# Kernel optimization log

Measured on AMD Instinct MI355X. Metric: run time of the kernel, lower is better.

The kernel has to match this reference:

```python
import jax, jax.numpy as jnp
import numpy as np

N_NODES = 100_000
N_EDGES = 1_200_000
D = 64


def setup_inputs() -> dict:
    key = jax.random.key(0)
    k1, k2, k3, k4, k5 = jax.random.split(key, 5)
    feat = jax.random.normal(k1, (N_NODES, D), dtype=jnp.float32)
    feat_0 = jax.random.normal(k2, (N_NODES, D), dtype=jnp.float32)
    std = 1.0 / np.sqrt(D)  # reset_parameters: uniform(-std, std), std = 1/sqrt(out_size)
    weight = jax.random.uniform(k3, (D, D), dtype=jnp.float32, minval=-std, maxval=std)
    src = jax.random.randint(k4, (N_EDGES,), 0, N_NODES, dtype=jnp.int32)
    dst = jax.random.randint(k5, (N_EDGES,), 0, N_NODES, dtype=jnp.int32)
    return {
        "feat": feat,
        "feat_0": feat_0,
        "weight": weight,
        "src": src,
        "dst": dst,
        "alpha": jnp.float32(0.1),
        "lamda": jnp.float32(0.5),
        "layer": 1,
    }


def reference(feat, feat_0, weight, src, dst, alpha, lamda, layer):
    # beta = log(lamda / layer + 1)
    beta = jnp.log(lamda / layer + 1.0)
    # in-degrees from destination endpoints, clamped at 1 (as in DGL path)
    degs = jax.ops.segment_sum(
        jnp.ones_like(dst, dtype=feat.dtype), dst, num_segments=N_NODES
    )
    norm = jnp.maximum(degs, 1.0) ** -0.5  # [N]
    norm = norm[:, None]  # [N, 1]
    # symmetric degree-normalized SpMM: D^{-1/2} A D^{-1/2} X via copy_u + sum
    h = feat * norm
    h = jax.ops.segment_sum(h[src], dst, num_segments=N_NODES)  # scatter-add over edges
    h = h * norm
    # GCNII combination: initial residual + identity mapping
    feat_sum = h * (1.0 - alpha) + feat_0 * alpha
    rst = (1.0 - beta) * feat_sum + beta * (feat_sum @ weight)
    return rst
```

## Files before the change

kernel.cpp:

```cpp
#include <hip/hip_runtime.h>
#include <hip/hip_fp16.h>

#define DDIM 64
#define MAXNS 2048
#define PART_TPB 256
#define PART_EPT 16
#define PART_EPB (PART_TPB * PART_EPT)

__device__ __forceinline__ float atomAddF(float* p, float v) {
    return unsafeAtomicAdd(p, v);
}


__global__ void slice_count_kernel(const int* __restrict__ dst, int* __restrict__ sliceCnt,
                                   int nE, int NS) {
    __shared__ int lh[MAXNS];
    int t = threadIdx.x;
    int blockBase = blockIdx.x * PART_EPB;
    for (int i = t; i < NS; i += PART_TPB) lh[i] = 0;
    __syncthreads();
    #pragma unroll
    for (int c = 0; c < 4; ++c) {
        int e0 = blockBase + (c * PART_TPB + t) * 4;
        if (e0 + 3 < nE) {
            int4 b = *(const int4*)(dst + e0);
            atomicAdd(&lh[b.x >> 8], 1); atomicAdd(&lh[b.y >> 8], 1);
            atomicAdd(&lh[b.z >> 8], 1); atomicAdd(&lh[b.w >> 8], 1);
        } else {
            for (int j = 0; j < 4; ++j) {
                int e = e0 + j;
                if (e < nE) atomicAdd(&lh[dst[e] >> 8], 1);
            }
        }
    }
    __syncthreads();
    for (int i = t; i < NS; i += PART_TPB)
        if (lh[i]) atomicAdd(&sliceCnt[i], lh[i]);
}

__global__ void slice_scan_wp_kernel(int* __restrict__ scnt, int* __restrict__ sbase,
                                     int NS, int nE,
                                     const float* __restrict__ W, const float* __restrict__ lamda_p,
                                     const int* __restrict__ layer_p, float* __restrict__ Wp) {
    __shared__ int sdata[512];
    int t = threadIdx.x;
    int base = t * 4;
    int v[4];
    #pragma unroll
    for (int j = 0; j < 4; ++j) {
        int idx = base + j;
        v[j] = (idx < NS) ? scnt[idx] : 0;
    }
    int local = v[0] + v[1] + v[2] + v[3];
    sdata[t] = local;
    __syncthreads();
    for (int off = 1; off < 512; off <<= 1) {
        int y = (t >= off) ? sdata[t - off] : 0;
        __syncthreads();
        sdata[t] += y;
        __syncthreads();
    }
    int run = sdata[t] - local;
    #pragma unroll
    for (int j = 0; j < 4; ++j) {
        int idx = base + j;
        if (idx < NS) { sbase[idx] = run; scnt[idx] = run; }
        run += v[j];
    }
    if (t == 0) sbase[NS] = nE;

    float lam = lamda_p[0];
    int lb = layer_p[0];
    float layerf = (lb > 0 && lb < (1 << 23)) ? (float)lb : __int_as_float(lb);
    float beta = logf(lam / layerf + 1.0f);
    for (int i = t; i < DDIM * DDIM; i += 512) {
        int k = i >> 6, d = i & 63;
        float w = beta * W[i];
        if (k == d) w += (1.0f - beta);
        Wp[i] = w;
    }
}

__global__ void partition_kernel(const int* __restrict__ src, const int* __restrict__ dst,
                                 int* __restrict__ cursor, unsigned* __restrict__ staging,
                                 int nE, int NS) {
    __shared__ int lh[MAXNS];
    __shared__ int lbase[MAXNS];
    int t = threadIdx.x;
    int blockBase = blockIdx.x * PART_EPB;
    for (int i = t; i < NS; i += PART_TPB) lh[i] = 0;
    __syncthreads();

    int se[PART_EPT]; int de[PART_EPT];
    #pragma unroll
    for (int c = 0; c < 4; ++c) {
        int e0 = blockBase + (c * PART_TPB + t) * 4;
        if (e0 + 3 < nE) {
            int4 a = *(const int4*)(src + e0);
            int4 b = *(const int4*)(dst + e0);
            se[4*c+0] = a.x; se[4*c+1] = a.y; se[4*c+2] = a.z; se[4*c+3] = a.w;
            de[4*c+0] = b.x; de[4*c+1] = b.y; de[4*c+2] = b.z; de[4*c+3] = b.w;
        } else {
            #pragma unroll
            for (int j = 0; j < 4; ++j) {
                int e = e0 + j;
                se[4*c+j] = (e < nE) ? src[e] : 0;
                de[4*c+j] = (e < nE) ? dst[e] : -1;
            }
        }
    }
    #pragma unroll
    for (int k = 0; k < PART_EPT; ++k)
        if (de[k] >= 0) atomicAdd(&lh[de[k] >> 8], 1);
    __syncthreads();
    for (int i = t; i < NS; i += PART_TPB) {
        int c = lh[i];
        if (c) lbase[i] = atomicAdd(&cursor[i], c);
        lh[i] = 0;
    }
    __syncthreads();
    #pragma unroll
    for (int k = 0; k < PART_EPT; ++k) {
        int d = de[k];
        if (d >= 0) {
            int sl = d >> 8;
            int off = atomicAdd(&lh[sl], 1);
            staging[lbase[sl] + off] = ((unsigned)se[k] << 8) | (unsigned)(d & 255);
        }
    }
}

__global__ void bin_fill_kernel(const unsigned* __restrict__ staging, const int* __restrict__ sbase,
                                int* __restrict__ degI, float* __restrict__ normv,
                                int* __restrict__ row_end, int* __restrict__ eidx, int nN) {
    __shared__ int cnt[256];
    __shared__ int pos[256];
    int s = blockIdx.x;
    int t = threadIdx.x;
    int b0 = sbase[s], b1 = sbase[s + 1];
    cnt[t] = 0;
    __syncthreads();
    for (int j = b0 + t; j < b1; j += 256) {
        unsigned p = staging[j];
        atomicAdd(&cnt[p & 255], 1);
    }
    __syncthreads();
    int c = cnt[t];
    pos[t] = c;
    __syncthreads();
    for (int off = 1; off < 256; off <<= 1) {
        int y = (t >= off) ? pos[t - off] : 0;
        __syncthreads();
        pos[t] += y;
        __syncthreads();
    }
    int inc = pos[t];
    int exc = inc - c;
    int node = (s << 8) + t;
    if (node < nN) {
        degI[node] = c;
        normv[node] = rsqrtf(fmaxf((float)c, 1.0f));
        row_end[node] = b0 + inc;
    }
    pos[t] = b0 + exc;
    __syncthreads();
    for (int j = b0 + t; j < b1; j += 256) {
        unsigned p = staging[j];
        int q = atomicAdd(&pos[p & 255], 1);
        eidx[q] = (int)(p >> 8);
    }
}

__global__ void scale_kernel(const float4* __restrict__ feat4, const float* __restrict__ normv,
                             uint2* __restrict__ featS2, int nN) {
    int b = blockIdx.x, t = threadIdx.x;
    int node = b * 16 + (t >> 4);
    int r = t & 15;
    if (node < nN) {
        float nv = normv[node];
        float4 v = feat4[(size_t)node * 16 + r];
        __half2 h0 = __floats2half2_rn(v.x * nv, v.y * nv);
        __half2 h1 = __floats2half2_rn(v.z * nv, v.w * nv);
        uint2 u;
        u.x = *(unsigned*)&h0;
        u.y = *(unsigned*)&h1;
        featS2[(size_t)node * 16 + r] = u;
    }
}


__global__ void deg_int_kernel(const int* __restrict__ dst, int* __restrict__ degI, int nE) {
    int i = blockIdx.x * blockDim.x + threadIdx.x;
    int base = i * 4;
    if (base + 3 < nE) {
        int4 d = *(const int4*)(dst + base);
        atomicAdd(&degI[d.x], 1); atomicAdd(&degI[d.y], 1);
        atomicAdd(&degI[d.z], 1); atomicAdd(&degI[d.w], 1);
    } else {
        for (int j = base; j < nE; ++j) atomicAdd(&degI[dst[j]], 1);
    }
}

#define SCAN_BLOCK 256
#define SCAN_CHUNK 1024

__global__ void scan1_kernel(const int* __restrict__ degI, int* __restrict__ row_start,
                             float* __restrict__ normv, int* __restrict__ blockSums, int nN) {
    __shared__ int sdata[SCAN_BLOCK];
    int t = threadIdx.x;
    int base = blockIdx.x * SCAN_CHUNK + t * 4;
    int v[4];
    #pragma unroll
    for (int j = 0; j < 4; ++j) {
        int idx = base + j;
        v[j] = (idx < nN) ? degI[idx] : 0;
    }
    int local = v[0] + v[1] + v[2] + v[3];
    sdata[t] = local;
    __syncthreads();
    for (int off = 1; off < SCAN_BLOCK; off <<= 1) {
        int y = (t >= off) ? sdata[t - off] : 0;
        __syncthreads();
        sdata[t] += y;
        __syncthreads();
    }
    int inc = sdata[t];
    int exc = inc - local;
    if (t == SCAN_BLOCK - 1) blockSums[blockIdx.x] = inc;
    int run = exc;
    #pragma unroll
    for (int j = 0; j < 4; ++j) {
        int idx = base + j;
        if (idx < nN) {
            row_start[idx] = run;
            normv[idx] = rsqrtf(fmaxf((float)v[j], 1.0f));
        }
        run += v[j];
    }
}

__global__ void scan2_wp_kernel(int* __restrict__ blockSums, int nb,
                                const float* __restrict__ W, const float* __restrict__ lamda_p,
                                const int* __restrict__ layer_p, float* __restrict__ Wp) {
    __shared__ int sdata[SCAN_BLOCK];
    int t = threadIdx.x;
    int v = (t < nb) ? blockSums[t] : 0;
    sdata[t] = v;
    __syncthreads();
    for (int off = 1; off < SCAN_BLOCK; off <<= 1) {
        int y = (t >= off) ? sdata[t - off] : 0;
        __syncthreads();
        sdata[t] += y;
        __syncthreads();
    }
    if (t < nb) blockSums[t] = sdata[t] - v;

    float lam = lamda_p[0];
    int lb = layer_p[0];
    float layerf = (lb > 0 && lb < (1 << 23)) ? (float)lb : __int_as_float(lb);
    float beta = logf(lam / layerf + 1.0f);
    for (int i = t; i < DDIM * DDIM; i += SCAN_BLOCK) {
        int k = i >> 6, d = i & 63;
        float w = beta * W[i];
        if (k == d) w += (1.0f - beta);
        Wp[i] = w;
    }
}

__global__ void scan3_scale_kernel(int* __restrict__ row_start, const int* __restrict__ blockSums,
                                   const float4* __restrict__ feat4, const float* __restrict__ normv,
                                   uint2* __restrict__ featS2, int nN) {
    int b = blockIdx.x, t = threadIdx.x;
    int node = b * 16 + (t >> 4);
    int r = t & 15;
    if (node < nN) {
        float nv = normv[node];
        float4 v = feat4[(size_t)node * 16 + r];
        __half2 h0 = __floats2half2_rn(v.x * nv, v.y * nv);
        __half2 h1 = __floats2half2_rn(v.z * nv, v.w * nv);
        uint2 u;
        u.x = *(unsigned*)&h0;
        u.y = *(unsigned*)&h1;
        featS2[(size_t)node * 16 + r] = u;
    }
    if (t < 16) {
        int n2 = b * 16 + t;
        if (n2 < nN) row_start[n2] += blockSums[n2 >> 10];
    }
}

__global__ void scan3_kernel(int* __restrict__ row_start, const int* __restrict__ blockSums, int nN) {
    int i = blockIdx.x * blockDim.x + threadIdx.x;
    if (i < nN) row_start[i] += blockSums[i >> 10];
}

__global__ void fill_kernel(const int* __restrict__ src, const int* __restrict__ dst,
                            int* __restrict__ row_start, int* __restrict__ eidx, int nE) {
    int i = blockIdx.x * blockDim.x + threadIdx.x;
    int base = i * 4;
    if (base + 3 < nE) {
        int4 s = *(const int4*)(src + base);
        int4 d = *(const int4*)(dst + base);
        eidx[atomicAdd(&row_start[d.x], 1)] = s.x;
        eidx[atomicAdd(&row_start[d.y], 1)] = s.y;
        eidx[atomicAdd(&row_start[d.z], 1)] = s.z;
        eidx[atomicAdd(&row_start[d.w], 1)] = s.w;
    } else {
        for (int j = base; j < nE; ++j) {
            int tt = dst[j];
            int p = atomicAdd(&row_start[tt], 1);
            eidx[p] = src[j];
        }
    }
}

template<bool HALF>
__global__ void gather_kernel(const void* __restrict__ featv_, const float4* __restrict__ feat04,
                              const float* __restrict__ normv, const int* __restrict__ degI,
                              const int* __restrict__ row_end, const int* __restrict__ eidx,
                              const float* __restrict__ Wp, const float* __restrict__ alpha_p,
                              float4* __restrict__ out4, int nN) {
    __shared__ float4 sW[DDIM * 16];
    const float4* Wp4 = (const float4*)Wp;
    for (int i = threadIdx.x; i < DDIM * 16; i += blockDim.x) {
        sW[(i & ~15) | ((i & 15) ^ ((i >> 8) & 3))] = Wp4[i];
    }
    __syncthreads();

    const float4* featF = (const float4*)featv_;
    const uint2*  featH = (const uint2*)featv_;

    int lane = threadIdx.x & 63;
    int w = threadIdx.x >> 6;
    int g = lane >> 4;
    int r = lane & 15;
    float alpha = alpha_p[0];

    for (int n = blockIdx.x * 4 + w; n < nN; n += gridDim.x * 4) {
        int end = row_end[n];
        int deg = degI[n];
        int start = end - deg;

        float4 acc = make_float4(0.f, 0.f, 0.f, 0.f);

        for (int j0 = start; j0 < end; j0 += 64) {
            int m = end - j0; if (m > 64) m = 64;
            int sIdx = 0;
            float nv = 1.0f;
            if (lane < m) {
                sIdx = eidx[j0 + lane];
                if (!HALF) nv = normv[sIdx];
            }
            int nt = (m + 3) >> 2;
            int t = 0;
            for (; t + 2 <= nt; t += 2) {
                int e0 = 4 * t + g, e1 = e0 + 4;
                int s0 = __shfl(sIdx, e0, 64);
                int s1 = __shfl(sIdx, e1, 64);
                float w0 = (e0 < m) ? 1.0f : 0.0f;
                float w1 = (e1 < m) ? 1.0f : 0.0f;
                if (HALF) {
                    uint2 ua = featH[(size_t)s0 * 16 + r];
                    uint2 ub = featH[(size_t)s1 * 16 + r];
                    float2 a0 = __half22float2(*(const __half2*)&ua.x);
                    float2 a1 = __half22float2(*(const __half2*)&ua.y);
                    float2 b0 = __half22float2(*(const __half2*)&ub.x);
                    float2 b1 = __half22float2(*(const __half2*)&ub.y);
                    acc.x = fmaf(a0.x, w0, acc.x); acc.y = fmaf(a0.y, w0, acc.y);
                    acc.z = fmaf(a1.x, w0, acc.z); acc.w = fmaf(a1.y, w0, acc.w);
                    acc.x = fmaf(b0.x, w1, acc.x); acc.y = fmaf(b0.y, w1, acc.y);
                    acc.z = fmaf(b1.x, w1, acc.z); acc.w = fmaf(b1.y, w1, acc.w);
                } else {
                    float ns0 = __shfl(nv, e0, 64);
                    float ns1 = __shfl(nv, e1, 64);
                    w0 *= ns0; w1 *= ns1;
                    float4 a = featF[(size_t)s0 * 16 + r];
                    float4 b = featF[(size_t)s1 * 16 + r];
                    acc.x = fmaf(a.x, w0, acc.x); acc.y = fmaf(a.y, w0, acc.y);
                    acc.z = fmaf(a.z, w0, acc.z); acc.w = fmaf(a.w, w0, acc.w);
                    acc.x = fmaf(b.x, w1, acc.x); acc.y = fmaf(b.y, w1, acc.y);
                    acc.z = fmaf(b.z, w1, acc.z); acc.w = fmaf(b.w, w1, acc.w);
                }
            }
            for (; t < nt; ++t) {
                int e = 4 * t + g;
                int s = __shfl(sIdx, e, 64);
                float w0 = (e < m) ? 1.0f : 0.0f;
                if (HALF) {
                    uint2 ua = featH[(size_t)s * 16 + r];
                    float2 a0 = __half22float2(*(const __half2*)&ua.x);
                    float2 a1 = __half22float2(*(const __half2*)&ua.y);
                    acc.x = fmaf(a0.x, w0, acc.x); acc.y = fmaf(a0.y, w0, acc.y);
                    acc.z = fmaf(a1.x, w0, acc.z); acc.w = fmaf(a1.y, w0, acc.w);
                } else {
                    float ns = __shfl(nv, e, 64);
                    w0 *= ns;
                    float4 a = featF[(size_t)s * 16 + r];
                    acc.x = fmaf(a.x, w0, acc.x); acc.y = fmaf(a.y, w0, acc.y);
                    acc.z = fmaf(a.z, w0, acc.z); acc.w = fmaf(a.w, w0, acc.w);
                }
            }
        }

        acc.x += __shfl_xor(acc.x, 16, 64); acc.y += __shfl_xor(acc.y, 16, 64);
        acc.z += __shfl_xor(acc.z, 16, 64); acc.w += __shfl_xor(acc.w, 16, 64);
        acc.x += __shfl_xor(acc.x, 32, 64); acc.y += __shfl_xor(acc.y, 32, 64);
        acc.z += __shfl_xor(acc.z, 32, 64); acc.w += __shfl_xor(acc.w, 32, 64);

        float sn = normv[n] * (1.0f - alpha);
        float4 f0 = feat04[(size_t)n * 16 + r];
        float4 fs;
        fs.x = fmaf(acc.x, sn, f0.x * alpha);
        fs.y = fmaf(acc.y, sn, f0.y * alpha);
        fs.z = fmaf(acc.z, sn, f0.z * alpha);
        fs.w = fmaf(acc.w, sn, f0.w * alpha);

        float4 res = make_float4(0.f, 0.f, 0.f, 0.f);
        #pragma unroll
        for (int kk = 0; kk < 16; ++kk) {
            int srcLane = 4 * g + (kk >> 2);
            float fscomp = ((kk & 3) == 0) ? fs.x : ((kk & 3) == 1) ? fs.y
                         : ((kk & 3) == 2) ? fs.z : fs.w;
            float fsk = __shfl(fscomp, srcLane, 64);
            float4 wv = sW[(16 * g + kk) * 16 + (r ^ g)];
            res.x = fmaf(fsk, wv.x, res.x);
            res.y = fmaf(fsk, wv.y, res.y);
            res.z = fmaf(fsk, wv.z, res.z);
            res.w = fmaf(fsk, wv.w, res.w);
        }
        res.x += __shfl_xor(res.x, 16, 64); res.y += __shfl_xor(res.y, 16, 64);
        res.z += __shfl_xor(res.z, 16, 64); res.w += __shfl_xor(res.w, 16, 64);
        res.x += __shfl_xor(res.x, 32, 64); res.y += __shfl_xor(res.y, 32, 64);
        res.z += __shfl_xor(res.z, 32, 64); res.w += __shfl_xor(res.w, 32, 64);

        if (g == 0) out4[(size_t)n * 16 + r] = res;
    }
}


__global__ void deg_kernel(const int* __restrict__ dst, float* __restrict__ degs, int nE) {
    int i = blockIdx.x * blockDim.x + threadIdx.x;
    if (i < nE) atomAddF(&degs[dst[i]], 1.0f);
}

__global__ void norm_kernel(float* degs, int nN) {
    int i = blockIdx.x * blockDim.x + threadIdx.x;
    if (i < nN) degs[i] = rsqrtf(fmaxf(degs[i], 1.0f));
}

__global__ void wp_kernel(const float* __restrict__ W, const float* __restrict__ lamda_p,
                          const int* __restrict__ layer_p, float* __restrict__ Wp) {
    int i = blockIdx.x * blockDim.x + threadIdx.x;
    if (i < DDIM * DDIM) {
        float lam = lamda_p[0];
        int lb = layer_p[0];
        float layerf = (lb > 0 && lb < (1 << 23)) ? (float)lb : __int_as_float(lb);
        float beta = logf(lam / layerf + 1.0f);
        int k = i >> 6, d = i & 63;
        float w = beta * W[i];
        if (k == d) w += (1.0f - beta);
        Wp[i] = w;
    }
}

__global__ void scatter_kernel(const float* __restrict__ feat, const float* __restrict__ norm,
                               const int* __restrict__ src, const int* __restrict__ dst,
                               float* __restrict__ accum, int nE) {
    long long gid = (long long)blockIdx.x * blockDim.x + threadIdx.x;
    int e = (int)(gid >> 6);
    int d = (int)(gid & 63);
    if (e < nE) {
        int s = src[e];
        int t = dst[e];
        float v = feat[(size_t)s * DDIM + d] * norm[s];
        atomAddF(&accum[(size_t)t * DDIM + d], v);
    }
}

__global__ void final_kernel(float* __restrict__ out, const float* __restrict__ feat0,
                             const float* __restrict__ norm, const float* __restrict__ Wp,
                             const float* __restrict__ alpha_p, int nN) {
    __shared__ float sW[DDIM * DDIM];
    for (int i = threadIdx.x; i < DDIM * DDIM; i += blockDim.x) sW[i] = Wp[i];
    __syncthreads();
    float alpha = alpha_p[0];
    int lane = threadIdx.x & 63;
    int w = threadIdx.x >> 6;
    int wavesPerBlock = blockDim.x >> 6;
    int nGroups = (nN + wavesPerBlock - 1) / wavesPerBlock;
    for (int gi = blockIdx.x; gi < nGroups; gi += gridDim.x) {
        int n = gi * wavesPerBlock + w;
        bool valid = n < nN;
        float fs = 0.0f;
        if (valid) {
            fs = out[(size_t)n * DDIM + lane] * norm[n] * (1.0f - alpha)
               + feat0[(size_t)n * DDIM + lane] * alpha;
        }
        float acc = 0.0f;
        #pragma unroll
        for (int k = 0; k < DDIM; ++k) {
            float fsk = __shfl(fs, k, 64);
            acc = fmaf(fsk, sW[k * DDIM + lane], acc);
        }
        if (valid) out[(size_t)n * DDIM + lane] = acc;
    }
}


static inline size_t align256(size_t x) { return (x + 255) & ~(size_t)255; }

extern "C" void kernel_launch(void* const* d_in, const int* in_sizes, int n_in,
                              void* d_out, int out_size, void* d_ws, size_t ws_size,
                              hipStream_t stream) {
    const float* feat  = (const float*)d_in[0];
    const float* feat0 = (const float*)d_in[1];
    const float* W     = (const float*)d_in[2];
    const int*   src   = (const int*)d_in[3];
    const int*   dst   = (const int*)d_in[4];
    const float* alpha = (const float*)d_in[5];
    const float* lamda = (const float*)d_in[6];
    const int*   layer = (const int*)d_in[7];
    float* out = (float*)d_out;

    int nN = in_sizes[0] / DDIM;
    int nE = in_sizes[3];
    int NS = (nN + 255) >> 8;
    int nb = (nN + SCAN_CHUNK - 1) / SCAN_CHUNK;

    size_t off = 0;
    size_t o_degI  = off; off += align256((size_t)nN * 4);
    size_t o_norm  = off; off += align256((size_t)nN * 4);
    size_t o_rowe  = off; off += align256((size_t)nN * 4);
    size_t o_sbase = off; off += align256((size_t)(NS + 1) * 4);
    size_t o_scnt  = off; off += align256((size_t)NS * 4);
    size_t o_wp    = off; off += align256((size_t)DDIM * DDIM * 4);
    size_t o_eidx  = off; off += align256((size_t)nE * 4);
    size_t base_sz = off;
    size_t o_featS = off; off += align256((size_t)nN * DDIM * 2);
    size_t need_t1 = off;
    size_t o_stag2 = base_sz;
    size_t need_t2 = base_sz + align256((size_t)nE * 4);

    bool newok = (NS >= 1 && NS <= MAXNS && nN <= (1 << 23));
    bool t1ok  = newok && ws_size >= need_t1 && ((size_t)nE * 4 <= (size_t)nN * DDIM * 2);
    bool t2ok  = newok && ws_size >= need_t2;

    if (t1ok || t2ok) {
        int*      degI  = (int*)  ((char*)d_ws + o_degI);
        float*    normv = (float*)((char*)d_ws + o_norm);
        int*      rowe  = (int*)  ((char*)d_ws + o_rowe);
        int*      sbase = (int*)  ((char*)d_ws + o_sbase);
        int*      scnt  = (int*)  ((char*)d_ws + o_scnt);
        float*    Wp    = (float*)((char*)d_ws + o_wp);
        int*      eidx  = (int*)  ((char*)d_ws + o_eidx);
        unsigned* stag  = (unsigned*)((char*)d_ws + (t1ok ? o_featS : o_stag2));
        float*    featS = (float*)((char*)d_ws + o_featS);

        hipMemsetAsync(scnt, 0, (size_t)NS * 4, stream);
        int pblocks = (nE + PART_EPB - 1) / PART_EPB;
        if (pblocks < 1) pblocks = 1;
        slice_count_kernel<<<pblocks, PART_TPB, 0, stream>>>(dst, scnt, nE, NS);
        slice_scan_wp_kernel<<<1, 512, 0, stream>>>(scnt, sbase, NS, nE, W, lamda, layer, Wp);
        partition_kernel<<<pblocks, PART_TPB, 0, stream>>>(src, dst, scnt, stag, nE, NS);
        bin_fill_kernel<<<NS, 256, 0, stream>>>(stag, sbase, degI, normv, rowe, eidx, nN);

        int gblocks = (nN + 3) / 4;
        if (gblocks > 4096) gblocks = 4096;
        if (t1ok) {
            scale_kernel<<<(nN + 15) / 16, 256, 0, stream>>>(
                (const float4*)feat, normv, (uint2*)featS, nN);
            gather_kernel<true><<<gblocks, 256, 0, stream>>>(
                (const void*)featS, (const float4*)feat0, normv, degI, rowe, eidx,
                Wp, alpha, (float4*)out, nN);
        } else {
            gather_kernel<false><<<gblocks, 256, 0, stream>>>(
                (const void*)feat, (const float4*)feat0, normv, degI, rowe, eidx,
                Wp, alpha, (float4*)out, nN);
        }
        return;
    }

    off = 0;
    size_t f_degI = off;      off += align256((size_t)nN * 4);
    size_t f_norm = off;      off += align256((size_t)nN * 4);
    size_t f_rows = off;      off += align256((size_t)nN * 4);
    size_t f_bsum = off;      off += align256((size_t)nb * 4);
    size_t f_wp   = off;      off += align256((size_t)DDIM * DDIM * 4);
    size_t f_eidx = off;      off += align256((size_t)nE * 4);
    size_t need_csr = off;
    size_t f_featS = off;     off += align256((size_t)nN * DDIM * 2);
    size_t need_full = off;

    if (ws_size >= need_csr && nb <= SCAN_BLOCK) {
        int*   degI  = (int*)  ((char*)d_ws + f_degI);
        float* normv = (float*)((char*)d_ws + f_norm);
        int*   rows  = (int*)  ((char*)d_ws + f_rows);
        int*   bsum  = (int*)  ((char*)d_ws + f_bsum);
        float* Wp    = (float*)((char*)d_ws + f_wp);
        int*   eidx  = (int*)  ((char*)d_ws + f_eidx);
        bool scaled = (ws_size >= need_full);
        float* featS = (float*)((char*)d_ws + f_featS);

        hipMemsetAsync(degI, 0, (size_t)nN * 4, stream);
        int e4blocks = ((nE + 3) / 4 + 255) / 256;
        deg_int_kernel<<<e4blocks, 256, 0, stream>>>(dst, degI, nE);
        scan1_kernel<<<nb, SCAN_BLOCK, 0, stream>>>(degI, rows, normv, bsum, nN);
        scan2_wp_kernel<<<1, SCAN_BLOCK, 0, stream>>>(bsum, nb, W, lamda, layer, Wp);
        if (scaled) {
            scan3_scale_kernel<<<(nN + 15) / 16, 256, 0, stream>>>(
                rows, bsum, (const float4*)feat, normv, (uint2*)featS, nN);
        } else {
            scan3_kernel<<<(nN + 255) / 256, 256, 0, stream>>>(rows, bsum, nN);
        }
        fill_kernel<<<e4blocks, 256, 0, stream>>>(src, dst, rows, eidx, nE);

        int gblocks = (nN + 3) / 4;
        if (gblocks > 4096) gblocks = 4096;
        if (scaled) {
            gather_kernel<true><<<gblocks, 256, 0, stream>>>(
                (const void*)featS, (const float4*)feat0, normv, degI, rows, eidx,
                Wp, alpha, (float4*)out, nN);
        } else {
            gather_kernel<false><<<gblocks, 256, 0, stream>>>(
                (const void*)feat, (const float4*)feat0, normv, degI, rows, eidx,
                Wp, alpha, (float4*)out, nN);
        }
    } else {
        float* degs = (float*)d_ws;
        size_t degs_bytes_al = align256((size_t)nN * 4);
        float* Wp = (float*)((char*)d_ws + degs_bytes_al);

        hipMemsetAsync(out, 0, (size_t)out_size * sizeof(float), stream);
        hipMemsetAsync(degs, 0, (size_t)nN * sizeof(float), stream);

        deg_kernel<<<(nE + 255) / 256, 256, 0, stream>>>(dst, degs, nE);
        norm_kernel<<<(nN + 255) / 256, 256, 0, stream>>>(degs, nN);
        wp_kernel<<<(DDIM * DDIM + 255) / 256, 256, 0, stream>>>(W, lamda, layer, Wp);

        long long tot = (long long)nE * DDIM;
        int sblocks = (int)((tot + 255) / 256);
        scatter_kernel<<<sblocks, 256, 0, stream>>>(feat, degs, src, dst, out, nE);
        final_kernel<<<2048, 256, 0, stream>>>(out, feat0, degs, Wp, alpha, nN);
    }
}
```

Measured before the change: 132.9 us.

## Gather eight edges per wave step with 16-byte half loads and 4-way unroll

Remaps the gather so each group of 8 lanes covers one 64-wide row, with each lane loading 16 bytes (8 halves) instead of 8. Each wave step now processes 8 edges instead of 4, and the inner loop is unrolled 4-way to keep more loads in flight. The 64x64 weight epilogue is reworked for the new lane mapping with a different shared-memory swizzle, and the grid cap is raised. The wider loads and extra accumulators raise register pressure and add a third shuffle-reduction stage.

```diff
diff --git a/kernel.cpp b/kernel.cpp
--- a/kernel.cpp
+++ b/kernel.cpp
@@ -323,17 +323,18 @@
     __shared__ float4 sW[DDIM * 16];
     const float4* Wp4 = (const float4*)Wp;
     for (int i = threadIdx.x; i < DDIM * 16; i += blockDim.x) {
-        sW[(i & ~15) | ((i & 15) ^ ((i >> 8) & 3))] = Wp4[i];
+        int k = i >> 4, c = i & 15;
+        sW[k * 16 + ((c + 2 * (k >> 3)) & 15)] = Wp4[i];
     }
     __syncthreads();
 
     const float4* featF = (const float4*)featv_;
-    const uint2*  featH = (const uint2*)featv_;
+    const uint4*  featH = (const uint4*)featv_;
 
     int lane = threadIdx.x & 63;
     int w = threadIdx.x >> 6;
-    int g = lane >> 4;
-    int r = lane & 15;
+    int g = lane >> 3;
+    int r = lane & 7;
     float alpha = alpha_p[0];
 
     for (int n = blockIdx.x * 4 + w; n < nN; n += gridDim.x * 4) {
@@ -341,7 +342,8 @@
         int deg = degI[n];
         int start = end - deg;
 
-        float4 acc = make_float4(0.f, 0.f, 0.f, 0.f);
+        float4 accA = make_float4(0.f, 0.f, 0.f, 0.f);
+        float4 accB = make_float4(0.f, 0.f, 0.f, 0.f);
 
         for (int j0 = start; j0 < end; j0 += 64) {
             int m = end - j0; if (m > 64) m = 64;
@@ -351,89 +353,127 @@
                 sIdx = eidx[j0 + lane];
                 if (!HALF) nv = normv[sIdx];
             }
-            int nt = (m + 3) >> 2;
+            int nt = (m + 7) >> 3;
             int t = 0;
+            for (; t + 4 <= nt; t += 4) {
+                int e0 = 8*t + g, e1 = e0 + 8, e2 = e0 + 16, e3 = e0 + 24;
+                int s0 = __shfl(sIdx, e0, 64);
+                int s1 = __shfl(sIdx, e1, 64);
+                int s2 = __shfl(sIdx, e2, 64);
+                int s3 = __shfl(sIdx, e3, 64);
+                float w0 = (e0 < m) ? 1.0f : 0.0f;
+                float w1 = (e1 < m) ? 1.0f : 0.0f;
+                float w2 = (e2 < m) ? 1.0f : 0.0f;
+                float w3 = (e3 < m) ? 1.0f : 0.0f;
+                if (HALF) {
+                    uint4 u0 = featH[(size_t)s0 * 8 + r];
+                    uint4 u1 = featH[(size_t)s1 * 8 + r];
+                    uint4 u2 = featH[(size_t)s2 * 8 + r];
+                    uint4 u3 = featH[(size_t)s3 * 8 + r];
+                    #define ACC_H(u, ww) { \
+                        float2 p0 = __half22float2(*(const __half2*)&(u).x); \
+                        float2 p1 = __half22float2(*(const __half2*)&(u).y); \
+                        float2 p2 = __half22float2(*(const __half2*)&(u).z); \
+                        float2 p3 = __half22float2(*(const __half2*)&(u).w); \
+                        accA.x = fmaf(p0.x, ww, accA.x); accA.y = fmaf(p0.y, ww, accA.y); \
+                        accA.z = fmaf(p1.x, ww, accA.z); accA.w = fmaf(p1.y, ww, accA.w); \
+                        accB.x = fmaf(p2.x, ww, accB.x); accB.y = fmaf(p2.y, ww, accB.y); \
+                        accB.z = fmaf(p3.x, ww, accB.z); accB.w = fmaf(p3.y, ww, accB.w); }
+                    ACC_H(u0, w0) ACC_H(u1, w1) ACC_H(u2, w2) ACC_H(u3, w3)
+                } else {
+                    w0 *= __shfl(nv, e0, 64); w1 *= __shfl(nv, e1, 64);
+                    w2 *= __shfl(nv, e2, 64); w3 *= __shfl(nv, e3, 64);
+                    float4 a0 = featF[(size_t)s0 * 16 + 2*r], a1 = featF[(size_t)s0 * 16 + 2*r + 1];
+                    float4 b0 = featF[(size_t)s1 * 16 + 2*r], b1 = featF[(size_t)s1 * 16 + 2*r + 1];
+                    float4 c0 = featF[(size_t)s2 * 16 + 2*r], c1 = featF[(size_t)s2 * 16 + 2*r + 1];
+                    float4 d0 = featF[(size_t)s3 * 16 + 2*r], d1 = featF[(size_t)s3 * 16 + 2*r + 1];
+                    #define ACC_F(x0, x1, ww) { \
+                        accA.x = fmaf((x0).x, ww, accA.x); accA.y = fmaf((x0).y, ww, accA.y); \
+                        accA.z = fmaf((x0).z, ww, accA.z); accA.w = fmaf((x0).w, ww, accA.w); \
+                        accB.x = fmaf((x1).x, ww, accB.x); accB.y = fmaf((x1).y, ww, accB.y); \
+                        accB.z = fmaf((x1).z, ww, accB.z); accB.w = fmaf((x1).w, ww, accB.w); }
+                    ACC_F(a0, a1, w0) ACC_F(b0, b1, w1) ACC_F(c0, c1, w2) ACC_F(d0, d1, w3)
+                }
+            }
             for (; t + 2 <= nt; t += 2) {
-                int e0 = 4 * t + g, e1 = e0 + 4;
+                int e0 = 8*t + g, e1 = e0 + 8;
                 int s0 = __shfl(sIdx, e0, 64);
                 int s1 = __shfl(sIdx, e1, 64);
                 float w0 = (e0 < m) ? 1.0f : 0.0f;
                 float w1 = (e1 < m) ? 1.0f : 0.0f;
                 if (HALF) {
-                    uint2 ua = featH[(size_t)s0 * 16 + r];
-                    uint2 ub = featH[(size_t)s1 * 16 + r];
-                    float2 a0 = __half22float2(*(const __half2*)&ua.x);
-                    float2 a1 = __half22float2(*(const __half2*)&ua.y);
-                    float2 b0 = __half22float2(*(const __half2*)&ub.x);
-                    float2 b1 = __half22float2(*(const __half2*)&ub.y);
-                    acc.x = fmaf(a0.x, w0, acc.x); acc.y = fmaf(a0.y, w0, acc.y);
-                    acc.z = fmaf(a1.x, w0, acc.z); acc.w = fmaf(a1.y, w0, acc.w);
-                    acc.x = fmaf(b0.x, w1, acc.x); acc.y = fmaf(b0.y, w1, acc.y);
-                    acc.z = fmaf(b1.x, w1, acc.z); acc.w = fmaf(b1.y, w1, acc.w);
+                    uint4 u0 = featH[(size_t)s0 * 8 + r];
+                    uint4 u1 = featH[(size_t)s1 * 8 + r];
+                    ACC_H(u0, w0) ACC_H(u1, w1)
                 } else {
-                    float ns0 = __shfl(nv, e0, 64);
-                    float ns1 = __shfl(nv, e1, 64);
-                    w0 *= ns0; w1 *= ns1;
-                    float4 a = featF[(size_t)s0 * 16 + r];
-                    float4 b = featF[(size_t)s1 * 16 + r];
-                    acc.x = fmaf(a.x, w0, acc.x); acc.y = fmaf(a.y, w0, acc.y);
-                    acc.z = fmaf(a.z, w0, acc.z); acc.w = fmaf(a.w, w0, acc.w);
-                    acc.x = fmaf(b.x, w1, acc.x); acc.y = fmaf(b.y, w1, acc.y);
-                    acc.z = fmaf(b.z, w1, acc.z); acc.w = fmaf(b.w, w1, acc.w);
+                    w0 *= __shfl(nv, e0, 64); w1 *= __shfl(nv, e1, 64);
+                    float4 a0 = featF[(size_t)s0 * 16 + 2*r], a1 = featF[(size_t)s0 * 16 + 2*r + 1];
+                    float4 b0 = featF[(size_t)s1 * 16 + 2*r], b1 = featF[(size_t)s1 * 16 + 2*r + 1];
+                    ACC_F(a0, a1, w0) ACC_F(b0, b1, w1)
                 }
             }
-            for (; t < nt; ++t) {
-                int e = 4 * t + g;
-                int s = __shfl(sIdx, e, 64);
-                float w0 = (e < m) ? 1.0f : 0.0f;
+            if (t < nt) {
+                int e0 = 8*t + g;
+                int s0 = __shfl(sIdx, e0, 64);
+                float w0 = (e0 < m) ? 1.0f : 0.0f;
                 if (HALF) {
-                    uint2 ua = featH[(size_t)s * 16 + r];
-                    float2 a0 = __half22float2(*(const __half2*)&ua.x);
-                    float2 a1 = __half22float2(*(const __half2*)&ua.y);
-                    acc.x = fmaf(a0.x, w0, acc.x); acc.y = fmaf(a0.y, w0, acc.y);
-                    acc.z = fmaf(a1.x, w0, acc.z); acc.w = fmaf(a1.y, w0, acc.w);
+                    uint4 u0 = featH[(size_t)s0 * 8 + r];
+                    ACC_H(u0, w0)
                 } else {
-                    float ns = __shfl(nv, e, 64);
-                    w0 *= ns;
-                    float4 a = featF[(size_t)s * 16 + r];
-                    acc.x = fmaf(a.x, w0, acc.x); acc.y = fmaf(a.y, w0, acc.y);
-                    acc.z = fmaf(a.z, w0, acc.z); acc.w = fmaf(a.w, w0, acc.w);
+                    w0 *= __shfl(nv, e0, 64);
+                    float4 a0 = featF[(size_t)s0 * 16 + 2*r], a1 = featF[(size_t)s0 * 16 + 2*r + 1];
+                    ACC_F(a0, a1, w0)
                 }
             }
         }
 
-        acc.x += __shfl_xor(acc.x, 16, 64); acc.y += __shfl_xor(acc.y, 16, 64);
-        acc.z += __shfl_xor(acc.z, 16, 64); acc.w += __shfl_xor(acc.w, 16, 64);
-        acc.x += __shfl_xor(acc.x, 32, 64); acc.y += __shfl_xor(acc.y, 32, 64);
-        acc.z += __shfl_xor(acc.z, 32, 64); acc.w += __shfl_xor(acc.w, 32, 64);
+        #define RED(acc) \
+            acc.x += __shfl_xor(acc.x, 8, 64);  acc.y += __shfl_xor(acc.y, 8, 64); \
+            acc.z += __shfl_xor(acc.z, 8, 64);  acc.w += __shfl_xor(acc.w, 8, 64); \
+            acc.x += __shfl_xor(acc.x, 16, 64); acc.y += __shfl_xor(acc.y, 16, 64); \
+            acc.z += __shfl_xor(acc.z, 16, 64); acc.w += __shfl_xor(acc.w, 16, 64); \
+            acc.x += __shfl_xor(acc.x, 32, 64); acc.y += __shfl_xor(acc.y, 32, 64); \
+            acc.z += __shfl_xor(acc.z, 32, 64); acc.w += __shfl_xor(acc.w, 32, 64);
+        RED(accA)
+        RED(accB)
 
         float sn = normv[n] * (1.0f - alpha);
-        float4 f0 = feat04[(size_t)n * 16 + r];
-        float4 fs;
-        fs.x = fmaf(acc.x, sn, f0.x * alpha);
-        fs.y = fmaf(acc.y, sn, f0.y * alpha);
-        fs.z = fmaf(acc.z, sn, f0.z * alpha);
-        fs.w = fmaf(acc.w, sn, f0.w * alpha);
-
-        float4 res = make_float4(0.f, 0.f, 0.f, 0.f);
+        float4 f0a = feat04[(size_t)n * 16 + 2*r];
+        float4 f0b = feat04[(size_t)n * 16 + 2*r + 1];
+        float4 fsA, fsB;
+        fsA.x = fmaf(accA.x, sn, f0a.x * alpha);
+        fsA.y = fmaf(accA.y, sn, f0a.y * alpha);
+        fsA.z = fmaf(accA.z, sn, f0a.z * alpha);
+        fsA.w = fmaf(accA.w, sn, f0a.w * alpha);
+        fsB.x = fmaf(accB.x, sn, f0b.x * alpha);
+        fsB.y = fmaf(accB.y, sn, f0b.y * alpha);
+        fsB.z = fmaf(accB.z, sn, f0b.z * alpha);
+        fsB.w = fmaf(accB.w, sn, f0b.w * alpha);
+
+        float4 resA = make_float4(0.f, 0.f, 0.f, 0.f);
+        float4 resB = make_float4(0.f, 0.f, 0.f, 0.f);
+        int cidx = (2*r + 2*g) & 15;
         #pragma unroll
-        for (int kk = 0; kk < 16; ++kk) {
-            int srcLane = 4 * g + (kk >> 2);
-            float fscomp = ((kk & 3) == 0) ? fs.x : ((kk & 3) == 1) ? fs.y
-                         : ((kk & 3) == 2) ? fs.z : fs.w;
-            float fsk = __shfl(fscomp, srcLane, 64);
-            float4 wv = sW[(16 * g + kk) * 16 + (r ^ g)];
-            res.x = fmaf(fsk, wv.x, res.x);
-            res.y = fmaf(fsk, wv.y, res.y);
-            res.z = fmaf(fsk, wv.z, res.z);
-            res.w = fmaf(fsk, wv.w, res.w);
-        }
-        res.x += __shfl_xor(res.x, 16, 64); res.y += __shfl_xor(res.y, 16, 64);
-        res.z += __shfl_xor(res.z, 16, 64); res.w += __shfl_xor(res.w, 16, 64);
-        res.x += __shfl_xor(res.x, 32, 64); res.y += __shfl_xor(res.y, 32, 64);
-        res.z += __shfl_xor(res.z, 32, 64); res.w += __shfl_xor(res.w, 32, 64);
-
-        if (g == 0) out4[(size_t)n * 16 + r] = res;
+        for (int kk = 0; kk < 8; ++kk) {
+            float fscomp = (kk == 0) ? fsA.x : (kk == 1) ? fsA.y : (kk == 2) ? fsA.z
+                         : (kk == 3) ? fsA.w : (kk == 4) ? fsB.x : (kk == 5) ? fsB.y
+                         : (kk == 6) ? fsB.z : fsB.w;
+            float fsk = __shfl(fscomp, g, 64);
+            int k4 = (8*g + kk) * 16;
+            float4 wv0 = sW[k4 + cidx];
+            float4 wv1 = sW[k4 + cidx + 1];
+            resA.x = fmaf(fsk, wv0.x, resA.x); resA.y = fmaf(fsk, wv0.y, resA.y);
+            resA.z = fmaf(fsk, wv0.z, resA.z); resA.w = fmaf(fsk, wv0.w, resA.w);
+            resB.x = fmaf(fsk, wv1.x, resB.x); resB.y = fmaf(fsk, wv1.y, resB.y);
+            resB.z = fmaf(fsk, wv1.z, resB.z); resB.w = fmaf(fsk, wv1.w, resB.w);
+        }
+        RED(resA)
+        RED(resB)
+
+        if (g == 0) {
+            out4[(size_t)n * 16 + 2*r]     = resA;
+            out4[(size_t)n * 16 + 2*r + 1] = resB;
+        }
     }
 }
 
@@ -565,7 +605,7 @@
         bin_fill_kernel<<<NS, 256, 0, stream>>>(stag, sbase, degI, normv, rowe, eidx, nN);
 
         int gblocks = (nN + 3) / 4;
-        if (gblocks > 4096) gblocks = 4096;
+        if (gblocks > 8192) gblocks = 8192;
         if (t1ok) {
             scale_kernel<<<(nN + 15) / 16, 256, 0, stream>>>(
                 (const float4*)feat, normv, (uint2*)featS, nN);
@@ -615,7 +655,7 @@
         fill_kernel<<<e4blocks, 256, 0, stream>>>(src, dst, rows, eidx, nE);
 
         int gblocks = (nN + 3) / 4;
-        if (gblocks > 4096) gblocks = 4096;
+        if (gblocks > 8192) gblocks = 8192;
         if (scaled) {
             gather_kernel<true><<<gblocks, 256, 0, stream>>>(
                 (const void*)featS, (const float4*)feat0, normv, degI, rows, eidx,
```

Result: slower. 147.1 us (+10.7%).
